# Kernel optimization log

Hardware: AMD Instinct MI355X
Metric: run time of the kernel (lower is better)

## Reference

```python
import jax, jax.numpy as jnp
import numpy as np

N = 100000       # num nodes
E = 1000000      # num edges
D_IN = 128       # input feature dim
D_H = 64         # hidden = output dim
EPS = 1e-5       # GraphNorm eps
SLOPE = 0.2      # LeakyReLU negative slope


def _glorot(key, shape):
    lim = float(np.sqrt(6.0 / (shape[0] + shape[1])))
    return jax.random.uniform(key, shape, jnp.float32, -lim, lim)


def setup_inputs() -> dict:
    key = jax.random.key(0)
    ks = jax.random.split(key, 6)
    return {
        "x": jax.random.normal(ks[0], (N, D_IN), jnp.float32),
        "edge_index": jax.random.randint(ks[1], (2, E), 0, N),
        "W_in": _glorot(ks[2], (D_IN, D_H)),
        "b_in": jnp.zeros((D_H,), jnp.float32),
        "W1": _glorot(ks[3], (D_H, D_H)),
        "b1": jnp.zeros((D_H,), jnp.float32),
        "gn1_alpha": jnp.ones((D_H,), jnp.float32),
        "gn1_gamma": jnp.ones((D_H,), jnp.float32),
        "gn1_beta": jnp.zeros((D_H,), jnp.float32),
        "W2": _glorot(ks[4], (D_H, D_H)),
        "b2": jnp.zeros((D_H,), jnp.float32),
        "gn2_alpha": jnp.ones((D_H,), jnp.float32),
        "gn2_gamma": jnp.ones((D_H,), jnp.float32),
        "gn2_beta": jnp.zeros((D_H,), jnp.float32),
    }


def gcn_conv(x, W, b, src, dst):
    # GCNConv with added self-loops and symmetric normalization:
    # out = D^{-1/2} (A + I) D^{-1/2} (x W) + b
    xw = x @ W                                                 # [N, D]
    ones = jnp.ones((src.shape[0],), x.dtype)
    deg = jax.ops.segment_sum(ones, dst, num_segments=x.shape[0]) + 1.0  # +1 self-loop
    dinv = jax.lax.rsqrt(deg)                                  # [N]
    coef = dinv[src] * dinv[dst]                               # [E]
    agg = jax.ops.segment_sum(xw[src] * coef[:, None], dst, num_segments=x.shape[0])
    return agg + xw * (dinv * dinv)[:, None] + b


def graph_norm(x, alpha, gamma, beta):
    # PyG GraphNorm over a single graph: per-feature mean/var over all nodes
    mean = jnp.mean(x, axis=0)
    c = x - alpha * mean
    var = jnp.mean(c * c, axis=0)
    return gamma * c * jax.lax.rsqrt(var + EPS) + beta


def reference(x, edge_index, W_in, b_in, W1, b1, gn1_alpha, gn1_gamma, gn1_beta,
              W2, b2, gn2_alpha, gn2_gamma, gn2_beta):
    src, dst = edge_index[0], edge_index[1]
    h = x @ W_in + b_in                                        # input projection
    h = graph_norm(gcn_conv(h, W1, b1, src, dst), gn1_alpha, gn1_gamma, gn1_beta)
    h = jnp.where(h > 0, h, SLOPE * h)                         # LeakyReLU(0.2); dropout=eval (identity)
    h = graph_norm(gcn_conv(h, W2, b2, src, dst), gn2_alpha, gn2_gamma, gn2_beta)
    return h                                                    # [N, D_H]
```

## Files before the change

### kernel.cpp

```cpp
#include <hip/hip_runtime.h>
#include <stdint.h>

#define N_NODES 100000
#define N_EDGES 1000000
#define D_IN 128
#define D_H 64
#define EPS 1e-5f
#define SLOPE 0.2f

typedef unsigned short u16;
typedef unsigned int u32;
typedef __attribute__((ext_vector_type(8))) short bf16x8;
typedef __attribute__((ext_vector_type(4))) float f32x4;

__device__ __forceinline__ float bf2f(u16 u) {
    union { u32 i; float f; } v; v.i = ((u32)u) << 16; return v.f;
}
__device__ __forceinline__ u16 f2bf(float f) {
    union { float f; u32 i; } v; v.f = f;
    u32 r = (v.i + 0x7fffu + ((v.i >> 16) & 1u)) >> 16;
    return (u16)r;
}
__device__ __forceinline__ bool is_f32(const void* flagp) {
    return *(const u32*)flagp == 0x3F800000u;
}
__device__ __forceinline__ float loadf(const void* p, size_t i, bool m) {
    return m ? ((const float*)p)[i] : bf2f(((const u16*)p)[i]);
}

__global__ void kprep(const void* __restrict__ W_in, const void* __restrict__ b_in,
                      const void* __restrict__ W1, const void* __restrict__ W2,
                      const void* __restrict__ flagp,
                      u16* __restrict__ WcT, u16* __restrict__ W2T,
                      float* __restrict__ bc, u16* __restrict__ xwb_pad)
{
    bool m = is_f32(flagp);
    int t = threadIdx.x;
    if (blockIdx.x < 64) {
        int c = blockIdx.x;
        __shared__ float w1c[D_H];
        if (t < D_H) w1c[t] = loadf(W1, t * D_H + c, m);
        __syncthreads();
        float acc = 0.f;
        #pragma unroll 8
        for (int j = 0; j < D_H; j++) acc += loadf(W_in, t * D_H + j, m) * w1c[j];
        WcT[c * D_IN + t] = f2bf(acc);
        if (t == 0) {
            float b = 0.f;
            for (int j = 0; j < D_H; j++) b += loadf(b_in, j, m) * w1c[j];
            bc[c] = b;
        }
        if (c == 0 && t < D_H) xwb_pad[(size_t)N_NODES * D_H + t] = 0;
    } else {
        int idx = (blockIdx.x - 64) * 128 + t;
        int n = idx >> 6, k = idx & 63;
        W2T[n * D_H + k] = f2bf(loadf(W2, k * D_H + n, m));
    }
}

__global__ void kfill(const int* __restrict__ ei, int* __restrict__ cnt,
                      int* __restrict__ bucket)
{
    int e = blockIdx.x * blockDim.x + threadIdx.x;
    if (e >= N_EDGES) return;
    int s = ei[e];
    int d = ei[N_EDGES + e];
    int slot = atomicAdd(&cnt[d], 1);
    if (slot < 64) bucket[(size_t)d * 64 + slot] = s;
}

__global__ __launch_bounds__(256) void kgemm1(const void* __restrict__ x,
        const u16* __restrict__ WcT, const float* __restrict__ bc,
        const int* __restrict__ cnt, const void* __restrict__ flagp,
        u16* __restrict__ xwb)
{
    bool m = is_f32(flagp);
    __shared__ __align__(16) u16 xs[64 * 136];
    __shared__ __align__(16) u16 WT[64 * 136];
    int tid = threadIdx.x;
    int row0 = blockIdx.x * 64;
    for (int i = tid; i < 64 * 32; i += 256) {
        int r = i >> 5, kq = (i & 31) * 4;
        *(ushort4*)(WT + r * 136 + kq) = *(const ushort4*)(WcT + r * D_IN + kq);
    }
    for (int i = tid; i < 64 * 32; i += 256) {
        int r = i >> 5, kq = (i & 31) * 4;
        int gr = row0 + r;
        ushort4 u = make_ushort4(0, 0, 0, 0);
        if (gr < N_NODES) {
            if (m) {
                float4 v = *(const float4*)((const float*)x + (size_t)gr * D_IN + kq);
                u = make_ushort4(f2bf(v.x), f2bf(v.y), f2bf(v.z), f2bf(v.w));
            } else {
                u = *(const ushort4*)((const u16*)x + (size_t)gr * D_IN + kq);
            }
        }
        *(ushort4*)(xs + r * 136 + kq) = u;
    }
    __syncthreads();
    int w = tid >> 6, L = tid & 63;
    int q = L >> 4, c = L & 15;
    f32x4 acc[4];
    #pragma unroll
    for (int ct = 0; ct < 4; ct++) {
        float b = bc[ct * 16 + c];
        acc[ct] = (f32x4){b, b, b, b};
    }
    const u16* ap = xs + (w * 16 + c) * 136 + q * 8;
    #pragma unroll
    for (int kk = 0; kk < 4; kk++) {
        bf16x8 af = *(const bf16x8*)(ap + kk * 32);
        #pragma unroll
        for (int ct = 0; ct < 4; ct++) {
            bf16x8 bfr = *(const bf16x8*)(WT + (ct * 16 + c) * 136 + kk * 32 + q * 8);
            acc[ct] = __builtin_amdgcn_mfma_f32_16x16x32_bf16(af, bfr, acc[ct], 0, 0, 0);
        }
    }
    #pragma unroll
    for (int r = 0; r < 4; r++) {
        int gr = row0 + w * 16 + q * 4 + r;
        if (gr < N_NODES) {
            float ds = rsqrtf((float)cnt[gr] + 1.0f);
            #pragma unroll
            for (int ct = 0; ct < 4; ct++)
                xwb[(size_t)gr * D_H + ct * 16 + c] = f2bf(acc[ct][r] * ds);
        }
    }
}

__global__ __launch_bounds__(256) void kagg(const u16* __restrict__ xwb,
        const int* __restrict__ cnt, const int* __restrict__ bucket,
        const void* __restrict__ bvec, const void* __restrict__ flagp,
        u16* __restrict__ ybuf, float* __restrict__ accum)
{
    bool m = is_f32(flagp);
    __shared__ float red_s[4][64], red_q[4][64];
    int tid = threadIdx.x;
    int wv = tid >> 6, L = tid & 63;
    int r = L >> 3, c = L & 7;
    int node0 = blockIdx.x * 32 + wv * 8;

    int cnt8 = cnt[node0 + (L & 7)];
    int tl = L >> 4, sl = L & 15;
    int raw0 = bucket[(size_t)(node0 + tl) * 64 + sl];
    int raw1 = bucket[(size_t)(node0 + 4 + tl) * 64 + sl];

    float bk[8];
    #pragma unroll
    for (int k = 0; k < 8; k++) bk[k] = loadf(bvec, c * 8 + k, m);

    const char* xb = (const char*)xwb;
    u32 coff = (u32)(c << 4);

    u32 offs[16];
    #pragma unroll
    for (int n = 0; n < 8; n++) {
        int dgn = min(__shfl(cnt8, n), 64);
        int ngl = node0 + n;
        #pragma unroll
        for (int g = 0; g < 2; g++) {
            int slot = g * 8 + r;
            int rw = __shfl((n < 4) ? raw0 : raw1, (n & 3) * 16 + slot);
            int sv = slot < dgn ? rw : (slot == dgn ? ngl : N_NODES);
            offs[n * 2 + g] = ((u32)sv << 7) | coff;
        }
    }

    uint4 q[16];
    __builtin_amdgcn_sched_barrier(0);
    #pragma unroll
    for (int i = 0; i < 16; i++) q[i] = *(const uint4*)(xb + offs[i]);
    __builtin_amdgcn_sched_barrier(0);

    float fA[8];
    #pragma unroll
    for (int n = 0; n < 8; n++) {
        float f[8] = {0.f, 0.f, 0.f, 0.f, 0.f, 0.f, 0.f, 0.f};
        #pragma unroll
        for (int g = 0; g < 2; g++) {
            uint4 qv = q[n * 2 + g];
            f[0] += __uint_as_float(qv.x << 16); f[1] += __uint_as_float(qv.x & 0xffff0000u);
            f[2] += __uint_as_float(qv.y << 16); f[3] += __uint_as_float(qv.y & 0xffff0000u);
            f[4] += __uint_as_float(qv.z << 16); f[5] += __uint_as_float(qv.z & 0xffff0000u);
            f[6] += __uint_as_float(qv.w << 16); f[7] += __uint_as_float(qv.w & 0xffff0000u);
        }
        #pragma unroll
        for (int k = 0; k < 8; k++) {
            f[k] += __shfl_xor(f[k], 8);
            f[k] += __shfl_xor(f[k], 16);
            f[k] += __shfl_xor(f[k], 32);
        }
        if (n == 0) {
            #pragma unroll
            for (int k = 0; k < 8; k++) fA[k] = (r == 0) ? f[k] : 0.f;
        } else {
            #pragma unroll
            for (int k = 0; k < 8; k++) if (r == n) fA[k] = f[k];
        }
    }

    int cvr = __shfl(cnt8, r);
    int dgr = min(cvr, 64);
    int nr = node0 + r;
    if (__any(dgr >= 16)) {
        for (int s = 16; s <= 64; s++) {
            if (!__any(s <= dgr)) break;
            if (s <= dgr) {
                int sv = (s < dgr) ? bucket[(size_t)nr * 64 + s] : nr;
                uint4 v = *(const uint4*)(xb + (((u32)sv << 7) | coff));
                fA[0] += __uint_as_float(v.x << 16); fA[1] += __uint_as_float(v.x & 0xffff0000u);
                fA[2] += __uint_as_float(v.y << 16); fA[3] += __uint_as_float(v.y & 0xffff0000u);
                fA[4] += __uint_as_float(v.z << 16); fA[5] += __uint_as_float(v.z & 0xffff0000u);
                fA[6] += __uint_as_float(v.w << 16); fA[7] += __uint_as_float(v.w & 0xffff0000u);
            }
        }
    }

    float dd = rsqrtf((float)cvr + 1.0f);
    float y[8];
    #pragma unroll
    for (int k = 0; k < 8; k++) y[k] = dd * fA[k] + bk[k];

    u32 p0 = (u32)f2bf(y[0]) | ((u32)f2bf(y[1]) << 16);
    u32 p1 = (u32)f2bf(y[2]) | ((u32)f2bf(y[3]) << 16);
    u32 p2 = (u32)f2bf(y[4]) | ((u32)f2bf(y[5]) << 16);
    u32 p3 = (u32)f2bf(y[6]) | ((u32)f2bf(y[7]) << 16);
    *(uint4*)((char*)ybuf + (size_t)nr * 128 + coff) = make_uint4(p0, p1, p2, p3);

    #pragma unroll
    for (int k = 0; k < 8; k++) {
        float s = y[k], qq = y[k] * y[k];
        s  += __shfl_xor(s, 8);  s  += __shfl_xor(s, 16);  s  += __shfl_xor(s, 32);
        qq += __shfl_xor(qq, 8); qq += __shfl_xor(qq, 16); qq += __shfl_xor(qq, 32);
        if (L < 8) { red_s[wv][c * 8 + k] = s; red_q[wv][c * 8 + k] = qq; }
    }
    __syncthreads();
    if (tid < 64) {
        atomicAdd(&accum[tid],      red_s[0][tid] + red_s[1][tid] + red_s[2][tid] + red_s[3][tid]);
        atomicAdd(&accum[64 + tid], red_q[0][tid] + red_q[1][tid] + red_q[2][tid] + red_q[3][tid]);
    }
}

__global__ __launch_bounds__(256) void kgemm2(const u16* __restrict__ y1b,
        const u16* __restrict__ W2T, const float* __restrict__ accum,
        const void* __restrict__ alpha, const void* __restrict__ gamma,
        const void* __restrict__ beta, const void* __restrict__ flagp,
        const int* __restrict__ cnt, u16* __restrict__ xwb)
{
    bool m = is_f32(flagp);
    __shared__ __align__(16) u16 hs[64 * 72];
    __shared__ __align__(16) u16 WT[64 * 72];
    __shared__ float aL[64], cL[64];
    int tid = threadIdx.x;
    if (tid < 64) {
        float mean = accum[tid] * (1.0f / N_NODES);
        float al = loadf(alpha, tid, m);
        float var = accum[64 + tid] * (1.0f / N_NODES) - mean * mean * al * (2.0f - al);
        var = fmaxf(var, 0.f);
        float a = loadf(gamma, tid, m) * rsqrtf(var + EPS);
        aL[tid] = a;
        cL[tid] = loadf(beta, tid, m) - a * al * mean;
    }
    for (int i = tid; i < 64 * 16; i += 256) {
        int r = i >> 4, kq = (i & 15) * 4;
        *(ushort4*)(WT + r * 72 + kq) = *(const ushort4*)(W2T + r * D_H + kq);
    }
    __syncthreads();
    int row0 = blockIdx.x * 64;
    for (int i = tid; i < 64 * 16; i += 256) {
        int r = i >> 4, kq = (i & 15) * 4;
        int gr = row0 + r;
        ushort4 u = make_ushort4(0, 0, 0, 0);
        if (gr < N_NODES) u = *(const ushort4*)(y1b + (size_t)gr * D_H + kq);
        float h0 = aL[kq + 0] * bf2f(u.x) + cL[kq + 0]; h0 = h0 > 0.f ? h0 : SLOPE * h0;
        float h1 = aL[kq + 1] * bf2f(u.y) + cL[kq + 1]; h1 = h1 > 0.f ? h1 : SLOPE * h1;
        float h2 = aL[kq + 2] * bf2f(u.z) + cL[kq + 2]; h2 = h2 > 0.f ? h2 : SLOPE * h2;
        float h3 = aL[kq + 3] * bf2f(u.w) + cL[kq + 3]; h3 = h3 > 0.f ? h3 : SLOPE * h3;
        *(ushort4*)(hs + r * 72 + kq) = make_ushort4(f2bf(h0), f2bf(h1), f2bf(h2), f2bf(h3));
    }
    __syncthreads();
    int w = tid >> 6, L = tid & 63;
    int q = L >> 4, c = L & 15;
    f32x4 acc[4] = {};
    const u16* ap = hs + (w * 16 + c) * 72 + q * 8;
    #pragma unroll
    for (int kk = 0; kk < 2; kk++) {
        bf16x8 af = *(const bf16x8*)(ap + kk * 32);
        #pragma unroll
        for (int ct = 0; ct < 4; ct++) {
            bf16x8 bfr = *(const bf16x8*)(WT + (ct * 16 + c) * 72 + kk * 32 + q * 8);
            acc[ct] = __builtin_amdgcn_mfma_f32_16x16x32_bf16(af, bfr, acc[ct], 0, 0, 0);
        }
    }
    #pragma unroll
    for (int r = 0; r < 4; r++) {
        int gr = row0 + w * 16 + q * 4 + r;
        if (gr < N_NODES) {
            float ds = rsqrtf((float)cnt[gr] + 1.0f);
            #pragma unroll
            for (int ct = 0; ct < 4; ct++)
                xwb[(size_t)gr * D_H + ct * 16 + c] = f2bf(acc[ct][r] * ds);
        }
    }
}

__global__ __launch_bounds__(256) void kout(const u16* __restrict__ y2b,
        const float* __restrict__ accum2, const void* __restrict__ alpha,
        const void* __restrict__ gamma, const void* __restrict__ beta,
        const void* __restrict__ flagp, void* __restrict__ out)
{
    bool m = is_f32(flagp);
    __shared__ float a2[64], c2[64];
    int tid = threadIdx.x;
    if (tid < 64) {
        float mean = accum2[tid] * (1.0f / N_NODES);
        float al = loadf(alpha, tid, m);
        float var = accum2[64 + tid] * (1.0f / N_NODES) - mean * mean * al * (2.0f - al);
        var = fmaxf(var, 0.f);
        float a = loadf(gamma, tid, m) * rsqrtf(var + EPS);
        a2[tid] = a;
        c2[tid] = loadf(beta, tid, m) - a * al * mean;
    }
    __syncthreads();
    int w0 = (blockIdx.x * 256 + tid) * 2;
    u32 v0 = ((const u32*)y2b)[w0];
    u32 v1 = ((const u32*)y2b)[w0 + 1];
    int f = (w0 * 2) & 63;
    float o0 = a2[f + 0] * __uint_as_float(v0 << 16)          + c2[f + 0];
    float o1 = a2[f + 1] * __uint_as_float(v0 & 0xffff0000u)  + c2[f + 1];
    float o2 = a2[f + 2] * __uint_as_float(v1 << 16)          + c2[f + 2];
    float o3 = a2[f + 3] * __uint_as_float(v1 & 0xffff0000u)  + c2[f + 3];
    if (m) {
        *(float4*)((float*)out + (size_t)w0 * 2) = make_float4(o0, o1, o2, o3);
    } else {
        u32 p0 = (u32)f2bf(o0) | ((u32)f2bf(o1) << 16);
        u32 p1 = (u32)f2bf(o2) | ((u32)f2bf(o3) << 16);
        *(uint2*)((u32*)out + w0) = make_uint2(p0, p1);
    }
}

extern "C" void kernel_launch(void* const* d_in, const int* in_sizes, int n_in,
                              void* d_out, int out_size, void* d_ws, size_t ws_size,
                              hipStream_t stream)
{
    const void* x    = d_in[0];
    const int*  ei   = (const int*)d_in[1];
    const void* W_in = d_in[2];
    const void* b_in = d_in[3];
    const void* W1   = d_in[4];
    const void* b1   = d_in[5];
    const void* gn1a = d_in[6];
    const void* gn1g = d_in[7];
    const void* gn1b = d_in[8];
    const void* W2   = d_in[9];
    const void* b2   = d_in[10];
    const void* gn2a = d_in[11];
    const void* gn2g = d_in[12];
    const void* gn2b = d_in[13];

    char* ws = (char*)d_ws;
    int*   cnt    = (int*)(ws + 0);
    float* accum  = (float*)(ws + 400000);
    float* bc     = (float*)(ws + 402048);
    u16*   WcT    = (u16*)(ws + 402432);
    u16*   W2T    = (u16*)(ws + 418816);
    int*   bucket = (int*)(ws + 1235200);
    u16*   bufA   = (u16*)(ws + 26835200);
    u16*   bufB   = (u16*)(ws + 39635456);

    hipMemsetAsync(ws, 0, 400000 + 1024, stream);

    kprep<<<96, 128, 0, stream>>>(W_in, b_in, W1, W2, gn1a, WcT, W2T, bc, bufA);
    kfill<<<(N_EDGES + 255) / 256, 256, 0, stream>>>(ei, cnt, bucket);
    kgemm1<<<(N_NODES + 63) / 64, 256, 0, stream>>>(x, WcT, bc, cnt, gn1a, bufA);
    kagg<<<N_NODES / 32, 256, 0, stream>>>(bufA, cnt, bucket, b1, gn1a, bufB, accum);
    kgemm2<<<(N_NODES + 63) / 64, 256, 0, stream>>>(bufB, W2T, accum, gn1a, gn1g, gn1b, gn1a, cnt, bufA);
    kagg<<<N_NODES / 32, 256, 0, stream>>>(bufA, cnt, bucket, b2, gn1a, bufB, accum + 128);
    kout<<<N_NODES * D_H / 1024, 256, 0, stream>>>(bufB, accum + 128, gn2a, gn2g, gn2b, gn1a, d_out);
}
```

Before: 399.0 us.

## Store node features in four 16-column slabs to localize gather traffic

Node feature buffers change from row-major [N,64] bf16 to four slabs of [N+1,16] bf16. The aggregation kernel then gathers one 32-byte segment per neighbor per pass, looping over slabs. Each pass touches a smaller working set (about 3.2 MB per slab), so gathered rows are more likely to hit in cache. In exchange, each edge needs four separate gather passes with smaller 4-byte loads, the bucket tail loop is repeated per slab, and the producer and consumer kernels must index the new layout.

Measured after the change: 413.8 us. +3.7%, slower.

```diff
diff --git a/kernel.cpp b/kernel.cpp
--- a/kernel.cpp
+++ b/kernel.cpp
@@ -12,6 +12,9 @@
 typedef unsigned int u32;
 typedef __attribute__((ext_vector_type(8))) short bf16x8;
 typedef __attribute__((ext_vector_type(4))) float f32x4;
+
+#define SLAB_U16 ((size_t)(N_NODES + 1) * 16)
+#define SLAB_D32 ((size_t)(N_NODES + 1) * 8)
 
 __device__ __forceinline__ float bf2f(u16 u) {
     union { u32 i; float f; } v; v.i = ((u32)u) << 16; return v.f;
@@ -50,7 +53,10 @@
             for (int j = 0; j < D_H; j++) b += loadf(b_in, j, m) * w1c[j];
             bc[c] = b;
         }
-        if (c == 0 && t < D_H) xwb_pad[(size_t)N_NODES * D_H + t] = 0;
+        if (c == 0 && t < D_H) {
+            int s = t >> 4, w = t & 15;
+            xwb_pad[(size_t)s * SLAB_U16 + (size_t)N_NODES * 16 + w] = 0;
+        }
     } else {
         int idx = (blockIdx.x - 64) * 128 + t;
         int n = idx >> 6, k = idx & 63;
@@ -123,7 +129,7 @@
             float ds = rsqrtf((float)cnt[gr] + 1.0f);
             #pragma unroll
             for (int ct = 0; ct < 4; ct++)
-                xwb[(size_t)gr * D_H + ct * 16 + c] = f2bf(acc[ct][r] * ds);
+                xwb[(size_t)ct * SLAB_U16 + (size_t)gr * 16 + c] = f2bf(acc[ct][r] * ds);
         }
     }
 }
@@ -145,14 +151,7 @@
     int raw0 = bucket[(size_t)(node0 + tl) * 64 + sl];
     int raw1 = bucket[(size_t)(node0 + 4 + tl) * 64 + sl];
 
-    float bk[8];
-    #pragma unroll
-    for (int k = 0; k < 8; k++) bk[k] = loadf(bvec, c * 8 + k, m);
-
-    const char* xb = (const char*)xwb;
-    u32 coff = (u32)(c << 4);
-
-    u32 offs[16];
+    int sv[16];
     #pragma unroll
     for (int n = 0; n < 8; n++) {
         int dgn = min(__shfl(cnt8, n), 64);
@@ -161,79 +160,67 @@
         for (int g = 0; g < 2; g++) {
             int slot = g * 8 + r;
             int rw = __shfl((n < 4) ? raw0 : raw1, (n & 3) * 16 + slot);
-            int sv = slot < dgn ? rw : (slot == dgn ? ngl : N_NODES);
-            offs[n * 2 + g] = ((u32)sv << 7) | coff;
-        }
-    }
-
-    uint4 q[16];
-    __builtin_amdgcn_sched_barrier(0);
-    #pragma unroll
-    for (int i = 0; i < 16; i++) q[i] = *(const uint4*)(xb + offs[i]);
-    __builtin_amdgcn_sched_barrier(0);
-
-    float fA[8];
-    #pragma unroll
-    for (int n = 0; n < 8; n++) {
-        float f[8] = {0.f, 0.f, 0.f, 0.f, 0.f, 0.f, 0.f, 0.f};
-        #pragma unroll
-        for (int g = 0; g < 2; g++) {
-            uint4 qv = q[n * 2 + g];
-            f[0] += __uint_as_float(qv.x << 16); f[1] += __uint_as_float(qv.x & 0xffff0000u);
-            f[2] += __uint_as_float(qv.y << 16); f[3] += __uint_as_float(qv.y & 0xffff0000u);
-            f[4] += __uint_as_float(qv.z << 16); f[5] += __uint_as_float(qv.z & 0xffff0000u);
-            f[6] += __uint_as_float(qv.w << 16); f[7] += __uint_as_float(qv.w & 0xffff0000u);
-        }
-        #pragma unroll
-        for (int k = 0; k < 8; k++) {
-            f[k] += __shfl_xor(f[k], 8);
-            f[k] += __shfl_xor(f[k], 16);
-            f[k] += __shfl_xor(f[k], 32);
-        }
-        if (n == 0) {
-            #pragma unroll
-            for (int k = 0; k < 8; k++) fA[k] = (r == 0) ? f[k] : 0.f;
-        } else {
-            #pragma unroll
-            for (int k = 0; k < 8; k++) if (r == n) fA[k] = f[k];
+            sv[n * 2 + g] = slot < dgn ? rw : (slot == dgn ? ngl : N_NODES);
         }
     }
 
     int cvr = __shfl(cnt8, r);
     int dgr = min(cvr, 64);
     int nr = node0 + r;
-    if (__any(dgr >= 16)) {
-        for (int s = 16; s <= 64; s++) {
-            if (!__any(s <= dgr)) break;
-            if (s <= dgr) {
-                int sv = (s < dgr) ? bucket[(size_t)nr * 64 + s] : nr;
-                uint4 v = *(const uint4*)(xb + (((u32)sv << 7) | coff));
-                fA[0] += __uint_as_float(v.x << 16); fA[1] += __uint_as_float(v.x & 0xffff0000u);
-                fA[2] += __uint_as_float(v.y << 16); fA[3] += __uint_as_float(v.y & 0xffff0000u);
-                fA[4] += __uint_as_float(v.z << 16); fA[5] += __uint_as_float(v.z & 0xffff0000u);
-                fA[6] += __uint_as_float(v.w << 16); fA[7] += __uint_as_float(v.w & 0xffff0000u);
+    float dd = rsqrtf((float)cvr + 1.0f);
+    bool anyrem = __any(dgr >= 16);
+
+    #pragma unroll
+    for (int p = 0; p < 4; p++) {
+        const u32* slab = (const u32*)xwb + (size_t)p * SLAB_D32;
+        u32 q[16];
+        #pragma unroll
+        for (int i = 0; i < 16; i++) q[i] = slab[(size_t)sv[i] * 8 + c];
+
+        float fA0 = 0.f, fA1 = 0.f;
+        #pragma unroll
+        for (int n = 0; n < 8; n++) {
+            u32 a = q[n * 2], b = q[n * 2 + 1];
+            float f0 = __uint_as_float(a << 16) + __uint_as_float(b << 16);
+            float f1 = __uint_as_float(a & 0xffff0000u) + __uint_as_float(b & 0xffff0000u);
+            f0 += __shfl_xor(f0, 8);  f1 += __shfl_xor(f1, 8);
+            f0 += __shfl_xor(f0, 16); f1 += __shfl_xor(f1, 16);
+            f0 += __shfl_xor(f0, 32); f1 += __shfl_xor(f1, 32);
+            if (r == n) { fA0 = f0; fA1 = f1; }
+        }
+
+        if (anyrem) {
+            for (int s = 16; s <= 64; s++) {
+                if (!__any(s <= dgr)) break;
+                if (s <= dgr) {
+                    int sv2 = (s < dgr) ? bucket[(size_t)nr * 64 + s] : nr;
+                    u32 v = slab[(size_t)sv2 * 8 + c];
+                    fA0 += __uint_as_float(v << 16);
+                    fA1 += __uint_as_float(v & 0xffff0000u);
+                }
             }
         }
-    }
-
-    float dd = rsqrtf((float)cvr + 1.0f);
-    float y[8];
-    #pragma unroll
-    for (int k = 0; k < 8; k++) y[k] = dd * fA[k] + bk[k];
-
-    u32 p0 = (u32)f2bf(y[0]) | ((u32)f2bf(y[1]) << 16);
-    u32 p1 = (u32)f2bf(y[2]) | ((u32)f2bf(y[3]) << 16);
-    u32 p2 = (u32)f2bf(y[4]) | ((u32)f2bf(y[5]) << 16);
-    u32 p3 = (u32)f2bf(y[6]) | ((u32)f2bf(y[7]) << 16);
-    *(uint4*)((char*)ybuf + (size_t)nr * 128 + coff) = make_uint4(p0, p1, p2, p3);
-
-    #pragma unroll
-    for (int k = 0; k < 8; k++) {
-        float s = y[k], qq = y[k] * y[k];
-        s  += __shfl_xor(s, 8);  s  += __shfl_xor(s, 16);  s  += __shfl_xor(s, 32);
-        qq += __shfl_xor(qq, 8); qq += __shfl_xor(qq, 16); qq += __shfl_xor(qq, 32);
-        if (L < 8) { red_s[wv][c * 8 + k] = s; red_q[wv][c * 8 + k] = qq; }
-    }
+
+        float b0 = loadf(bvec, p * 16 + 2 * c, m);
+        float b1 = loadf(bvec, p * 16 + 2 * c + 1, m);
+        float y0 = dd * fA0 + b0;
+        float y1 = dd * fA1 + b1;
+        ((u32*)ybuf)[(size_t)p * SLAB_D32 + (size_t)nr * 8 + c] =
+            (u32)f2bf(y0) | ((u32)f2bf(y1) << 16);
+
+        float s0 = y0, s1 = y1, q0 = y0 * y0, q1 = y1 * y1;
+        s0 += __shfl_xor(s0, 8);  s1 += __shfl_xor(s1, 8);
+        q0 += __shfl_xor(q0, 8);  q1 += __shfl_xor(q1, 8);
+        s0 += __shfl_xor(s0, 16); s1 += __shfl_xor(s1, 16);
+        q0 += __shfl_xor(q0, 16); q1 += __shfl_xor(q1, 16);
+        s0 += __shfl_xor(s0, 32); s1 += __shfl_xor(s1, 32);
+        q0 += __shfl_xor(q0, 32); q1 += __shfl_xor(q1, 32);
+        if (r == 0) {
+            red_s[wv][p * 16 + 2 * c] = s0;  red_s[wv][p * 16 + 2 * c + 1] = s1;
+            red_q[wv][p * 16 + 2 * c] = q0;  red_q[wv][p * 16 + 2 * c + 1] = q1;
+        }
+    }
+
     __syncthreads();
     if (tid < 64) {
         atomicAdd(&accum[tid],      red_s[0][tid] + red_s[1][tid] + red_s[2][tid] + red_s[3][tid]);
@@ -271,7 +258,10 @@
         int r = i >> 4, kq = (i & 15) * 4;
         int gr = row0 + r;
         ushort4 u = make_ushort4(0, 0, 0, 0);
-        if (gr < N_NODES) u = *(const ushort4*)(y1b + (size_t)gr * D_H + kq);
+        if (gr < N_NODES) {
+            int s = kq >> 4, off = kq & 15;
+            u = *(const ushort4*)(y1b + (size_t)s * SLAB_U16 + (size_t)gr * 16 + off);
+        }
         float h0 = aL[kq + 0] * bf2f(u.x) + cL[kq + 0]; h0 = h0 > 0.f ? h0 : SLOPE * h0;
         float h1 = aL[kq + 1] * bf2f(u.y) + cL[kq + 1]; h1 = h1 > 0.f ? h1 : SLOPE * h1;
         float h2 = aL[kq + 2] * bf2f(u.z) + cL[kq + 2]; h2 = h2 > 0.f ? h2 : SLOPE * h2;
@@ -299,7 +289,7 @@
             float ds = rsqrtf((float)cnt[gr] + 1.0f);
             #pragma unroll
             for (int ct = 0; ct < 4; ct++)
-                xwb[(size_t)gr * D_H + ct * 16 + c] = f2bf(acc[ct][r] * ds);
+                xwb[(size_t)ct * SLAB_U16 + (size_t)gr * 16 + c] = f2bf(acc[ct][r] * ds);
         }
     }
 }
@@ -322,20 +312,23 @@
         c2[tid] = loadf(beta, tid, m) - a * al * mean;
     }
     __syncthreads();
-    int w0 = (blockIdx.x * 256 + tid) * 2;
-    u32 v0 = ((const u32*)y2b)[w0];
-    u32 v1 = ((const u32*)y2b)[w0 + 1];
-    int f = (w0 * 2) & 63;
+    int gid = blockIdx.x * 256 + tid;
+    int nd = gid >> 4, q4 = gid & 15;
+    int s = q4 >> 2, pr = q4 & 3;
+    const u32* yp = (const u32*)y2b + (size_t)s * SLAB_D32 + (size_t)nd * 8 + pr * 2;
+    u32 v0 = yp[0];
+    u32 v1 = yp[1];
+    int f = q4 * 4;
     float o0 = a2[f + 0] * __uint_as_float(v0 << 16)          + c2[f + 0];
     float o1 = a2[f + 1] * __uint_as_float(v0 & 0xffff0000u)  + c2[f + 1];
     float o2 = a2[f + 2] * __uint_as_float(v1 << 16)          + c2[f + 2];
     float o3 = a2[f + 3] * __uint_as_float(v1 & 0xffff0000u)  + c2[f + 3];
     if (m) {
-        *(float4*)((float*)out + (size_t)w0 * 2) = make_float4(o0, o1, o2, o3);
+        *(float4*)((float*)out + (size_t)nd * 64 + f) = make_float4(o0, o1, o2, o3);
     } else {
         u32 p0 = (u32)f2bf(o0) | ((u32)f2bf(o1) << 16);
         u32 p1 = (u32)f2bf(o2) | ((u32)f2bf(o3) << 16);
-        *(uint2*)((u32*)out + w0) = make_uint2(p0, p1);
+        *(uint2*)((u32*)out + (size_t)nd * 32 + f / 2) = make_uint2(p0, p1);
     }
 }
 
@@ -376,5 +369,5 @@
     kagg<<<N_NODES / 32, 256, 0, stream>>>(bufA, cnt, bucket, b1, gn1a, bufB, accum);
     kgemm2<<<(N_NODES + 63) / 64, 256, 0, stream>>>(bufB, W2T, accum, gn1a, gn1g, gn1b, gn1a, cnt, bufA);
     kagg<<<N_NODES / 32, 256, 0, stream>>>(bufA, cnt, bucket, b2, gn1a, bufB, accum + 128);
-    kout<<<N_NODES * D_H / 1024, 256, 0, stream>>>(bufB, accum + 128, gn2a, gn2g, gn2b, gn1a, d_out);
-}
+    kout<<<N_NODES * 16 / 256, 256, 0, stream>>>(bufB, accum + 128, gn2a, gn2g, gn2b, gn1a, d_out);
+}
```
